# Performance work log

Hardware: AMD Instinct MI355X
Metric: run time of the kernel (lower is better)

The kernel has to match this reference:

```python
import jax
jax.config.update("jax_enable_x64", True)
import jax.numpy as jnp
import numpy as np

FMIX32_C1 = 2246822507
FMIX32_C2 = 3266489909
POS_C1 = 668265261
POS_C2 = 374761393
SEED = 608135816
TILE = 8192
N_WORDS = 67108864  # 64M uint32 words = 256 MB


def _fmix32(x):
    # MurmurHash3 fmix32 finalizer on uint32 (wrapping arithmetic)
    x = x ^ (x >> 16)
    x = x * jnp.uint32(FMIX32_C1)
    x = x ^ (x >> 13)
    x = x * jnp.uint32(FMIX32_C2)
    x = x ^ (x >> 16)
    return x


def _rotl32(x, r):
    return (x << r) | (x >> (32 - r))


def setup_inputs() -> dict:
    key = jax.random.key(0)
    input_words = jax.random.randint(key, (N_WORDS,), 0, 2**31 - 1, dtype=jnp.int32)
    return {"input_words": input_words}


def _hash_tiles(input_words):
    v = input_words.view(jnp.uint32) if input_words.dtype != jnp.uint32 else input_words
    v = jax.lax.bitcast_convert_type(input_words, jnp.uint32)
    n = v.shape[0]
    n_tiles = (n + TILE - 1) // TILE
    n_pad = n_tiles * TILE
    v = jnp.pad(v, (0, n_pad - n))  # padded words hash to 0 via mask below
    v = v.reshape(n_tiles, TILE)

    s1 = jnp.uint32(SEED & 0xFFFFFFFF)
    s2 = jnp.uint32((SEED * 2654435761 ^ 3735928559) & 0xFFFFFFFF)
    posA = jnp.uint32(POS_C1)
    posB = jnp.uint32(POS_C2)

    idx = jnp.arange(n_pad, dtype=jnp.uint32).reshape(n_tiles, TILE)
    m = idx < jnp.uint32(n)

    # Python precedence in the kernel: (iu*posA + s1) ^ rotl(iu, 15)
    p1 = (idx * posA + s1) ^ _rotl32(idx, 15)
    p2 = (idx * posB + s2) ^ _rotl32(idx, 13)

    k1 = jnp.where(m, _fmix32(v ^ p1), jnp.uint32(0))
    k2 = jnp.where(m, _fmix32(v ^ p2), jnp.uint32(0))

    h1 = jnp.sum(k1, axis=1, dtype=jnp.uint32)  # wrapping per-tile reduction
    h2 = jnp.sum(k2, axis=1, dtype=jnp.uint32)

    nbytes = jnp.uint32((n * 4) & 0xFFFFFFFF)
    h1 = _fmix32(h1 ^ nbytes)
    h2 = _fmix32(h2 ^ nbytes)

    out = (h1.astype(jnp.uint64) << 32) | h2.astype(jnp.uint64)
    return jax.lax.bitcast_convert_type(out, jnp.int64)  # torch returns int64


def reference(input_words) -> jnp.ndarray:
    return _hash_tiles(input_words)
```

## Files before the change

### kernel.cpp

```cpp
#include <hip/hip_runtime.h>
#include <stdint.h>


static constexpr uint32_t FMIX_C1 = 2246822507u;
static constexpr uint32_t FMIX_C2 = 3266489909u;
static constexpr uint32_t POS_A   = 668265261u;
static constexpr uint32_t POS_B   = 374761393u;
static constexpr uint32_t S1      = 608135816u;
static constexpr uint32_t S2      = (608135816u * 2654435761u) ^ 3735928559u;

__device__ __forceinline__ uint32_t fmix32(uint32_t x) {
    x ^= x >> 16;
    x *= FMIX_C1;
    x ^= x >> 13;
    x *= FMIX_C2;
    x ^= x >> 16;
    return x;
}

__device__ __forceinline__ uint32_t rotl32(uint32_t x, uint32_t r) {
    return (x << r) | (x >> (32u - r));
}

template <bool PAIRS>
__global__ __launch_bounds__(256) void hash_tiles_kernel(
        const uint32_t* __restrict__ in, uint32_t* __restrict__ out,
        uint32_t nbytes) {
    const uint32_t gid  = blockIdx.x * 256u + threadIdx.x;
    const uint32_t tile = gid >> 6;
    const uint32_t lane = threadIdx.x & 63u;
    const uint32_t base = tile << 13;

    const uint4* __restrict__ vin =
        reinterpret_cast<const uint4*>(in + base) + lane;

    uint32_t acc1 = 0u, acc2 = 0u;
    uint32_t iw = base + (lane << 2);
    uint32_t mA = iw * POS_A + S1;
    uint32_t mB = iw * POS_B + S2;
    const uint32_t stepA = 256u * POS_A;
    const uint32_t stepB = 256u * POS_B;

    #pragma unroll 4
    for (int r = 0; r < 32; ++r) {
        uint4 v = vin[r << 6];
        #pragma unroll
        for (int j = 0; j < 4; ++j) {
            uint32_t w = (j == 0) ? v.x : (j == 1) ? v.y : (j == 2) ? v.z : v.w;
            uint32_t ij = iw + (uint32_t)j;
            if (PAIRS) {
                uint32_t p1 = (mA + (uint32_t)j * POS_A) ^ rotl32(ij, 15);
                acc1 += fmix32(w ^ p1);
            }
            uint32_t p2 = (mB + (uint32_t)j * POS_B) ^ rotl32(ij, 13);
            acc2 += fmix32(w ^ p2);
        }
        iw += 256u; mA += stepA; mB += stepB;
    }

    #pragma unroll
    for (int off = 32; off > 0; off >>= 1) {
        if (PAIRS) acc1 += (uint32_t)__shfl_xor((int)acc1, off, 64);
        acc2 += (uint32_t)__shfl_xor((int)acc2, off, 64);
    }

    if (lane == 0) {
        uint32_t h2 = fmix32(acc2 ^ nbytes);
        if (PAIRS) {
            uint32_t h1 = fmix32(acc1 ^ nbytes);
            uint2 packed;
            packed.x = h2;
            packed.y = h1;
            reinterpret_cast<uint2*>(out)[tile] = packed;
        } else {
            out[tile] = h2;
        }
    }
}

extern "C" void kernel_launch(void* const* d_in, const int* in_sizes, int n_in,
                              void* d_out, int out_size, void* d_ws, size_t ws_size,
                              hipStream_t stream) {
    const uint32_t* in = (const uint32_t*)d_in[0];
    uint32_t* out = (uint32_t*)d_out;

    const uint32_t n       = (uint32_t)in_sizes[0];
    const uint32_t n_tiles = n >> 13;
    const uint32_t nbytes  = n << 2;

    dim3 block(256);
    dim3 grid(n_tiles >> 2);

    if ((uint32_t)out_size >= 2u * n_tiles) {
        hipLaunchKernelGGL(hash_tiles_kernel<true>, grid, block, 0, stream,
                           in, out, nbytes);
    } else {
        hipLaunchKernelGGL(hash_tiles_kernel<false>, grid, block, 0, stream,
                           in, out, nbytes);
    }
}
```

Baseline: 349.8 us.

## Assign one tile per block and issue all eight loads upfront

```diff
diff --git a/kernel.cpp b/kernel.cpp
--- a/kernel.cpp
+++ b/kernel.cpp
@@ -18,44 +18,45 @@
     return x;
 }
 
-__device__ __forceinline__ uint32_t rotl32(uint32_t x, uint32_t r) {
-    return (x << r) | (x >> (32u - r));
+__device__ __forceinline__ uint32_t rotl32(uint32_t x, int r) {
+    return (x << r) | (x >> (32 - r));
 }
 
 template <bool PAIRS>
-__global__ __launch_bounds__(256) void hash_tiles_kernel(
+__global__ __launch_bounds__(256, 4) void hash_tiles_kernel(
         const uint32_t* __restrict__ in, uint32_t* __restrict__ out,
         uint32_t nbytes) {
-    const uint32_t gid  = blockIdx.x * 256u + threadIdx.x;
-    const uint32_t tile = gid >> 6;
-    const uint32_t lane = threadIdx.x & 63u;
+    const uint32_t tile = blockIdx.x;
+    const uint32_t t    = threadIdx.x;
     const uint32_t base = tile << 13;
+    const uint32_t iw0  = base + (t << 2);
 
     const uint4* __restrict__ vin =
-        reinterpret_cast<const uint4*>(in + base) + lane;
+        reinterpret_cast<const uint4*>(in + base) + t;
+
+    uint4 v[8];
+    #pragma unroll
+    for (int r = 0; r < 8; ++r) v[r] = vin[r << 8];
+
+    const uint32_t mA0 = iw0 * POS_A + S1;
+    const uint32_t mB0 = iw0 * POS_B + S2;
 
     uint32_t acc1 = 0u, acc2 = 0u;
-    uint32_t iw = base + (lane << 2);
-    uint32_t mA = iw * POS_A + S1;
-    uint32_t mB = iw * POS_B + S2;
-    const uint32_t stepA = 256u * POS_A;
-    const uint32_t stepB = 256u * POS_B;
-
-    #pragma unroll 4
-    for (int r = 0; r < 32; ++r) {
-        uint4 v = vin[r << 6];
+    #pragma unroll
+    for (int r = 0; r < 8; ++r) {
         #pragma unroll
         for (int j = 0; j < 4; ++j) {
-            uint32_t w = (j == 0) ? v.x : (j == 1) ? v.y : (j == 2) ? v.z : v.w;
-            uint32_t ij = iw + (uint32_t)j;
+            const uint32_t c = ((uint32_t)r << 10) + (uint32_t)j;
+            uint32_t w  = (j == 0) ? v[r].x : (j == 1) ? v[r].y
+                        : (j == 2) ? v[r].z : v[r].w;
+            uint32_t ij = iw0 + c;
             if (PAIRS) {
-                uint32_t p1 = (mA + (uint32_t)j * POS_A) ^ rotl32(ij, 15);
+                uint32_t p1 = (mA0 + c * POS_A) ^ rotl32(ij, 15);
                 acc1 += fmix32(w ^ p1);
             }
-            uint32_t p2 = (mB + (uint32_t)j * POS_B) ^ rotl32(ij, 13);
+            uint32_t p2 = (mB0 + c * POS_B) ^ rotl32(ij, 13);
             acc2 += fmix32(w ^ p2);
         }
-        iw += 256u; mA += stepA; mB += stepB;
     }
 
     #pragma unroll
@@ -64,10 +65,21 @@
         acc2 += (uint32_t)__shfl_xor((int)acc2, off, 64);
     }
 
-    if (lane == 0) {
-        uint32_t h2 = fmix32(acc2 ^ nbytes);
+    __shared__ uint32_t sp1[4];
+    __shared__ uint32_t sp2[4];
+    const uint32_t wid = t >> 6;
+    if ((t & 63u) == 0u) {
+        if (PAIRS) sp1[wid] = acc1;
+        sp2[wid] = acc2;
+    }
+    __syncthreads();
+
+    if (t == 0) {
+        uint32_t a2 = sp2[0] + sp2[1] + sp2[2] + sp2[3];
+        uint32_t h2 = fmix32(a2 ^ nbytes);
         if (PAIRS) {
-            uint32_t h1 = fmix32(acc1 ^ nbytes);
+            uint32_t a1 = sp1[0] + sp1[1] + sp1[2] + sp1[3];
+            uint32_t h1 = fmix32(a1 ^ nbytes);
             uint2 packed;
             packed.x = h2;
             packed.y = h1;
@@ -89,7 +101,7 @@
     const uint32_t nbytes  = n << 2;
 
     dim3 block(256);
-    dim3 grid(n_tiles >> 2);
+    dim3 grid(n_tiles);
 
     if ((uint32_t)out_size >= 2u * n_tiles) {
         hipLaunchKernelGGL(hash_tiles_kernel<true>, grid, block, 0, stream,
```

New measurement: 350.8 us. Within noise of the previous version (+0.3%).
